# Optimization experiments

Measured on AMD Instinct MI355X. Metric: run time of the kernel, lower is better.

## Reference

```python
import jax, jax.numpy as jnp
import numpy as np

N = 100000   # nodes
G = 128      # graphs for mean pool


def gcn_conv(x, edge_index, W, b, num_nodes):
    # PyG GCNConv (default): x' = D^-1/2 (A+I) D^-1/2 (x W) + b
    x = x @ W
    src, dst = edge_index[0], edge_index[1]
    loop = jnp.arange(num_nodes)
    src = jnp.concatenate([src, loop])
    dst = jnp.concatenate([dst, loop])
    ones = jnp.ones(src.shape[0], x.dtype)
    deg = jax.ops.segment_sum(ones, dst, num_segments=num_nodes)
    dinv = jnp.where(deg > 0, jax.lax.rsqrt(deg), 0.0)
    norm = dinv[src] * dinv[dst]            # [E+N]
    msg = x[src] * norm[:, None]            # gather + scale
    out = jax.ops.segment_sum(msg, dst, num_segments=num_nodes)  # scatter-add
    return out + b


def setup_inputs() -> dict:
    key = jax.random.key(0)
    ks = jax.random.split(key, 5)
    x = jax.random.normal(ks[0], (N, 128), jnp.float32)
    edge_index = jax.random.randint(ks[1], (2, 1600000), 0, N)
    batch = jnp.sort(jax.random.randint(ks[2], (N,), 0, G))
    W1 = jax.random.normal(ks[3], (128, 64), jnp.float32) / np.sqrt(128.0)
    b1 = jnp.zeros((64,), jnp.float32)
    W2 = jax.random.normal(ks[4], (64, 64), jnp.float32) / np.sqrt(64.0)
    b2 = jnp.zeros((64,), jnp.float32)
    return {"x": x, "edge_index": edge_index, "batch": batch,
            "W1": W1, "b1": b1, "W2": W2, "b2": b2}


def reference(x, edge_index, batch, W1, b1, W2, b2):
    h = gcn_conv(x, edge_index, W1, b1, N)
    h = jax.nn.relu(h)  # dropout is identity in eval mode
    h = gcn_conv(h, edge_index, W2, b2, N)
    # global_mean_pool over graph ids
    s = jax.ops.segment_sum(h, batch, num_segments=G)
    cnt = jax.ops.segment_sum(jnp.ones((N,), h.dtype), batch, num_segments=G)
    return s / jnp.maximum(cnt, 1.0)[:, None]   # [G, hidden2]
```

## Files before the change

### kernel.cpp

```cpp
#include <hip/hip_runtime.h>
#include <hip/hip_fp16.h>

#define SLOTS 64

__global__ __launch_bounds__(256) void fill_pad(const int* __restrict__ src,
                                                const int* __restrict__ dst, int E, int N,
                                                int* __restrict__ deg,
                                                int* __restrict__ colpad, int chunks) {
  int range = blockIdx.x & 7;
  int chunk = blockIdx.x >> 3;
  int per = (N + 7) >> 3;
  int lo = range * per, hi = min(N, lo + per);
  int e0 = (int)((long long)chunk * E / chunks);
  int e1 = (int)((long long)(chunk + 1) * E / chunks);
  for (int e = e0 + (int)threadIdx.x; e < e1; e += 256) {
    int d = dst[e];
    if (d >= lo && d < hi) {
      int p = atomicAdd(&deg[d], 1);
      if (p < SLOTS) colpad[(size_t)p * N + d] = src[e];
    }
  }
}

__global__ __launch_bounds__(256) void calc_dinv(const int* __restrict__ deg,
                                                 float* __restrict__ dinv, int N) {
  int i = blockIdx.x * 256 + threadIdx.x;
  if (i < N) dinv[i] = rsqrtf((float)(deg[i] + 1));
}

template <int K, typename Tin>
__global__ __launch_bounds__(256) void gemm_dinv(const Tin* __restrict__ in,
                                                 const float* __restrict__ W,
                                                 const float* __restrict__ dinv,
                                                 __half* __restrict__ out, int N, int tiles) {
  constexpr int K4 = K / 4;
  __shared__ float4 Ws4[64][K4];
  __shared__ float Xs[32][K];
  int t = threadIdx.x;
  for (int j = t; j < 64 * K4; j += 256) {
    int c = j / K4, k4 = j % K4;
    float4 v;
    v.x = W[(4 * k4 + 0) * 64 + c];
    v.y = W[(4 * k4 + 1) * 64 + c];
    v.z = W[(4 * k4 + 2) * 64 + c];
    v.w = W[(4 * k4 + 3) * 64 + c];
    Ws4[c][k4 ^ (c & 7)] = v;
  }
  __syncthreads();
  int c0 = t & 31, rg = t >> 5;
  for (int tile = blockIdx.x; tile < tiles; tile += gridDim.x) {
    int row0 = tile * 32;
    if constexpr (sizeof(Tin) == 4) {
      for (int j = t; j < 32 * K4; j += 256) {
        int r = j / K4, k4 = j % K4;
        int rr = row0 + r;
        float4 v = (rr < N) ? *(const float4*)&in[(size_t)rr * K + 4 * k4]
                            : make_float4(0.f, 0.f, 0.f, 0.f);
        *(float4*)&Xs[r][4 * k4] = v;
      }
    } else {
      for (int j = t; j < 32 * (K / 2); j += 256) {
        int r = j / (K / 2), kk = j % (K / 2);
        int rr = row0 + r;
        float2 v = make_float2(0.f, 0.f);
        if (rr < N) {
          __half2 h = *(const __half2*)&in[(size_t)rr * K + 2 * kk];
          v = __half22float2(h);
        }
        Xs[r][2 * kk] = v.x;
        Xs[r][2 * kk + 1] = v.y;
      }
    }
    __syncthreads();
    float acc[4][2];
#pragma unroll
    for (int r = 0; r < 4; ++r) { acc[r][0] = 0.f; acc[r][1] = 0.f; }
#pragma unroll 4
    for (int k4 = 0; k4 < K4; ++k4) {
      float4 w0 = Ws4[c0][k4 ^ (c0 & 7)];
      float4 w1 = Ws4[c0 + 32][k4 ^ (c0 & 7)];
#pragma unroll
      for (int r = 0; r < 4; ++r) {
        float4 xv = *(const float4*)&Xs[rg * 4 + r][4 * k4];
        acc[r][0] = fmaf(xv.w, w0.w, fmaf(xv.z, w0.z, fmaf(xv.y, w0.y, fmaf(xv.x, w0.x, acc[r][0]))));
        acc[r][1] = fmaf(xv.w, w1.w, fmaf(xv.z, w1.z, fmaf(xv.y, w1.y, fmaf(xv.x, w1.x, acc[r][1]))));
      }
    }
#pragma unroll
    for (int r = 0; r < 4; ++r) {
      int row = row0 + rg * 4 + r;
      if (row < N) {
        float s = dinv[row];
        out[(size_t)row * 64 + c0]      = __float2half(acc[r][0] * s);
        out[(size_t)row * 64 + c0 + 32] = __float2half(acc[r][1] * s);
      }
    }
    __syncthreads();
  }
}

__global__ __launch_bounds__(256) void aggregate(const __half* __restrict__ g,
                                                 const int* __restrict__ deg_arr,
                                                 const int* __restrict__ colpad,
                                                 const float* __restrict__ dinv,
                                                 const float* __restrict__ bias,
                                                 const int* __restrict__ batch,
                                                 __half* __restrict__ out,
                                                 float* __restrict__ poolsum,
                                                 float* __restrict__ poolcnt,
                                                 int N, int mode) {
  int lane = threadIdx.x & 63;
  int wave = blockIdx.x * 4 + (threadIdx.x >> 6);
  int nwaves = gridDim.x * 4;
  int per = (N + nwaves - 1) / nwaves;
  int n0 = wave * per, n1 = min(N, n0 + per);
  if (n0 >= n1) return;
  float b = bias[lane];
  int cur = mode ? batch[n0] : 0;
  float pacc = 0.f, pcnt = 0.f;
  const int* myplane = colpad + (size_t)lane * N;
  for (int node = n0; node < n1; ++node) {
    int deg = min(deg_arr[node], SLOTS);
    int nb = (lane < deg) ? myplane[node] : 0;
    float a0 = __half2float(g[(size_t)node * 64 + lane]);
    float a1 = 0.f, a2 = 0.f, a3 = 0.f;
    float a4 = 0.f, a5 = 0.f, a6 = 0.f, a7 = 0.f;
    int j = 0;
    for (; j + 7 < deg; j += 8) {
      int s0 = __shfl(nb, j, 64);
      int s1 = __shfl(nb, j + 1, 64);
      int s2 = __shfl(nb, j + 2, 64);
      int s3 = __shfl(nb, j + 3, 64);
      int s4 = __shfl(nb, j + 4, 64);
      int s5 = __shfl(nb, j + 5, 64);
      int s6 = __shfl(nb, j + 6, 64);
      int s7 = __shfl(nb, j + 7, 64);
      a0 += __half2float(g[(size_t)s0 * 64 + lane]);
      a1 += __half2float(g[(size_t)s1 * 64 + lane]);
      a2 += __half2float(g[(size_t)s2 * 64 + lane]);
      a3 += __half2float(g[(size_t)s3 * 64 + lane]);
      a4 += __half2float(g[(size_t)s4 * 64 + lane]);
      a5 += __half2float(g[(size_t)s5 * 64 + lane]);
      a6 += __half2float(g[(size_t)s6 * 64 + lane]);
      a7 += __half2float(g[(size_t)s7 * 64 + lane]);
    }
    for (; j + 3 < deg; j += 4) {
      int s0 = __shfl(nb, j, 64);
      int s1 = __shfl(nb, j + 1, 64);
      int s2 = __shfl(nb, j + 2, 64);
      int s3 = __shfl(nb, j + 3, 64);
      a0 += __half2float(g[(size_t)s0 * 64 + lane]);
      a1 += __half2float(g[(size_t)s1 * 64 + lane]);
      a2 += __half2float(g[(size_t)s2 * 64 + lane]);
      a3 += __half2float(g[(size_t)s3 * 64 + lane]);
    }
    for (; j < deg; ++j) a0 += __half2float(g[(size_t)__shfl(nb, j, 64) * 64 + lane]);
    float r = dinv[node] * (((a0 + a1) + (a2 + a3)) + ((a4 + a5) + (a6 + a7))) + b;
    if (mode == 0) {
      out[(size_t)node * 64 + lane] = __float2half(fmaxf(r, 0.f));
    } else {
      int bg = batch[node];
      if (bg != cur) {
        atomicAdd(&poolsum[cur * 64 + lane], pacc);
        if (lane == 0) atomicAdd(&poolcnt[cur], pcnt);
        pacc = 0.f; pcnt = 0.f; cur = bg;
      }
      pacc += r; pcnt += 1.f;
    }
  }
  if (mode) {
    atomicAdd(&poolsum[cur * 64 + lane], pacc);
    if (lane == 0) atomicAdd(&poolcnt[cur], pcnt);
  }
}

__global__ __launch_bounds__(256) void finalize(const float* __restrict__ poolsum,
                                                const float* __restrict__ poolcnt,
                                                float* __restrict__ out, int Gn) {
  int i = blockIdx.x * 256 + threadIdx.x;
  if (i < Gn * 64) {
    float c = poolcnt[i >> 6];
    out[i] = poolsum[i] / fmaxf(c, 1.f);
  }
}

extern "C" void kernel_launch(void* const* d_in, const int* in_sizes, int n_in,
                              void* d_out, int out_size, void* d_ws, size_t ws_size,
                              hipStream_t stream) {
  const float* x   = (const float*)d_in[0];
  const int* ei    = (const int*)d_in[1];
  const int* batch = (const int*)d_in[2];
  const float* W1  = (const float*)d_in[3];
  const float* b1  = (const float*)d_in[4];
  const float* W2  = (const float*)d_in[5];
  const float* b2  = (const float*)d_in[6];
  float* out = (float*)d_out;

  int N  = in_sizes[2];
  int E  = in_sizes[1] / 2;
  int Gn = out_size / 64;

  char* ws = (char*)d_ws;
  size_t off = 0;
  auto alloc = [&](size_t bytes) -> void* {
    void* p = ws + off;
    off = (off + bytes + 255) & ~(size_t)255;
    return p;
  };
  int* deg       = (int*)alloc(4ull * N);
  float* poolsum = (float*)alloc(4ull * Gn * 64);
  float* poolcnt = (float*)alloc(4ull * Gn);
  size_t zero_bytes = off;
  int* colpad    = (int*)alloc(4ull * (size_t)N * SLOTS);
  float* dinv    = (float*)alloc(4ull * N);
  __half* gbuf   = (__half*)alloc(2ull * (size_t)N * 64);
  __half* ybuf   = (__half*)alloc(2ull * (size_t)N * 64);
  (void)ws_size; (void)n_in;

  hipMemsetAsync(d_ws, 0, zero_bytes, stream);

  const int* srcv = ei;
  const int* dstv = ei + E;
  int tiles = (N + 31) / 32;

  fill_pad<<<8 * 256, 256, 0, stream>>>(srcv, dstv, E, N, deg, colpad, 256);
  calc_dinv<<<(N + 255) / 256, 256, 0, stream>>>(deg, dinv, N);

  gemm_dinv<128, float><<<1536, 256, 0, stream>>>(x, W1, dinv, gbuf, N, tiles);
  aggregate<<<2048, 256, 0, stream>>>(gbuf, deg, colpad, dinv, b1, batch, ybuf,
                                      nullptr, nullptr, N, 0);
  gemm_dinv<64, __half><<<1536, 256, 0, stream>>>(ybuf, W2, dinv, gbuf, N, tiles);
  aggregate<<<2048, 256, 0, stream>>>(gbuf, deg, colpad, dinv, b2, batch, nullptr,
                                      poolsum, poolcnt, N, 1);
  finalize<<<(Gn * 64 + 255) / 256, 256, 0, stream>>>(poolsum, poolcnt, out, Gn);
}
```

Measured before the change: 366.4 us.

## Replace scalar FP32 GEMM with fp16 MFMA 16x16x32 matrix-core kernel

Rewrites the dense feature-transform kernel to use the fp16 MFMA intrinsic instead of per-thread scalar FMA loops. The input rows and the transposed weights are staged in LDS as fp16 with padded rows, and each wave computes a 16x64 output slab. The tile grows to 64 rows and the launch uses one block per tile. The fp32 input features are now rounded to fp16 before the multiply, which lowers precision. The output stores are narrower scalar half writes with a different lane mapping.

Result: faster. 311.9 us (-14.9%).

```diff
diff --git a/kernel.cpp b/kernel.cpp
--- a/kernel.cpp
+++ b/kernel.cpp
@@ -2,6 +2,9 @@
 #include <hip/hip_fp16.h>
 
 #define SLOTS 64
+
+typedef _Float16 half8 __attribute__((ext_vector_type(8)));
+typedef float f32x4 __attribute__((ext_vector_type(4)));
 
 __global__ __launch_bounds__(256) void fill_pad(const int* __restrict__ src,
                                                 const int* __restrict__ dst, int E, int N,
@@ -29,70 +32,68 @@
 }
 
 template <int K, typename Tin>
-__global__ __launch_bounds__(256) void gemm_dinv(const Tin* __restrict__ in,
+__global__ __launch_bounds__(256) void gemm_mfma(const Tin* __restrict__ in,
                                                  const float* __restrict__ W,
                                                  const float* __restrict__ dinv,
-                                                 __half* __restrict__ out, int N, int tiles) {
-  constexpr int K4 = K / 4;
-  __shared__ float4 Ws4[64][K4];
-  __shared__ float Xs[32][K];
+                                                 __half* __restrict__ out,
+                                                 int N, int tiles) {
+  constexpr int LDK = K + 8;
+  __shared__ __align__(16) _Float16 As[64][LDK];
+  __shared__ __align__(16) _Float16 Wt[64][LDK];
   int t = threadIdx.x;
-  for (int j = t; j < 64 * K4; j += 256) {
-    int c = j / K4, k4 = j % K4;
-    float4 v;
-    v.x = W[(4 * k4 + 0) * 64 + c];
-    v.y = W[(4 * k4 + 1) * 64 + c];
-    v.z = W[(4 * k4 + 2) * 64 + c];
-    v.w = W[(4 * k4 + 3) * 64 + c];
-    Ws4[c][k4 ^ (c & 7)] = v;
-  }
-  __syncthreads();
-  int c0 = t & 31, rg = t >> 5;
+  for (int j = t; j < K * 64; j += 256) {
+    int k = j >> 6, c = j & 63;
+    Wt[c][k] = (_Float16)W[j];
+  }
+  int wave = t >> 6, lane = t & 63;
+  int arow = lane & 15;
+  int kgrp = lane >> 4;
+  constexpr int C8 = K / 8;
+
   for (int tile = blockIdx.x; tile < tiles; tile += gridDim.x) {
-    int row0 = tile * 32;
-    if constexpr (sizeof(Tin) == 4) {
-      for (int j = t; j < 32 * K4; j += 256) {
-        int r = j / K4, k4 = j % K4;
-        int rr = row0 + r;
-        float4 v = (rr < N) ? *(const float4*)&in[(size_t)rr * K + 4 * k4]
-                            : make_float4(0.f, 0.f, 0.f, 0.f);
-        *(float4*)&Xs[r][4 * k4] = v;
-      }
-    } else {
-      for (int j = t; j < 32 * (K / 2); j += 256) {
-        int r = j / (K / 2), kk = j % (K / 2);
-        int rr = row0 + r;
-        float2 v = make_float2(0.f, 0.f);
+    int row0 = tile * 64;
+    for (int j = t; j < 64 * C8; j += 256) {
+      int r = j / C8, k8 = (j % C8) * 8;
+      int rr = row0 + r;
+      if constexpr (sizeof(Tin) == 4) {
+        half8 h = (half8)((_Float16)0.f);
         if (rr < N) {
-          __half2 h = *(const __half2*)&in[(size_t)rr * K + 2 * kk];
-          v = __half22float2(h);
+          float4 v0 = *(const float4*)&in[(size_t)rr * K + k8];
+          float4 v1 = *(const float4*)&in[(size_t)rr * K + k8 + 4];
+          h[0] = (_Float16)v0.x; h[1] = (_Float16)v0.y;
+          h[2] = (_Float16)v0.z; h[3] = (_Float16)v0.w;
+          h[4] = (_Float16)v1.x; h[5] = (_Float16)v1.y;
+          h[6] = (_Float16)v1.z; h[7] = (_Float16)v1.w;
         }
-        Xs[r][2 * kk] = v.x;
-        Xs[r][2 * kk + 1] = v.y;
+        *(half8*)&As[r][k8] = h;
+      } else {
+        float4 v = make_float4(0.f, 0.f, 0.f, 0.f);
+        if (rr < N) v = *(const float4*)&in[(size_t)rr * K + k8];
+        *(float4*)&As[r][k8] = v;
       }
     }
     __syncthreads();
-    float acc[4][2];
-#pragma unroll
-    for (int r = 0; r < 4; ++r) { acc[r][0] = 0.f; acc[r][1] = 0.f; }
-#pragma unroll 4
-    for (int k4 = 0; k4 < K4; ++k4) {
-      float4 w0 = Ws4[c0][k4 ^ (c0 & 7)];
-      float4 w1 = Ws4[c0 + 32][k4 ^ (c0 & 7)];
+    f32x4 acc[4];
+#pragma unroll
+    for (int ct = 0; ct < 4; ++ct) acc[ct] = (f32x4)(0.f);
+#pragma unroll
+    for (int kk = 0; kk < K; kk += 32) {
+      half8 a = *(const half8*)&As[wave * 16 + arow][kk + kgrp * 8];
+#pragma unroll
+      for (int ct = 0; ct < 4; ++ct) {
+        half8 b = *(const half8*)&Wt[ct * 16 + arow][kk + kgrp * 8];
+        acc[ct] = __builtin_amdgcn_mfma_f32_16x16x32_f16(a, b, acc[ct], 0, 0, 0);
+      }
+    }
+#pragma unroll
+    for (int ct = 0; ct < 4; ++ct) {
 #pragma unroll
       for (int r = 0; r < 4; ++r) {
-        float4 xv = *(const float4*)&Xs[rg * 4 + r][4 * k4];
-        acc[r][0] = fmaf(xv.w, w0.w, fmaf(xv.z, w0.z, fmaf(xv.y, w0.y, fmaf(xv.x, w0.x, acc[r][0]))));
-        acc[r][1] = fmaf(xv.w, w1.w, fmaf(xv.z, w1.z, fmaf(xv.y, w1.y, fmaf(xv.x, w1.x, acc[r][1]))));
-      }
-    }
-#pragma unroll
-    for (int r = 0; r < 4; ++r) {
-      int row = row0 + rg * 4 + r;
-      if (row < N) {
-        float s = dinv[row];
-        out[(size_t)row * 64 + c0]      = __float2half(acc[r][0] * s);
-        out[(size_t)row * 64 + c0 + 32] = __float2half(acc[r][1] * s);
+        int row = row0 + wave * 16 + kgrp * 4 + r;
+        if (row < N) {
+          int col = ct * 16 + arow;
+          out[(size_t)row * 64 + col] = __float2half(acc[ct][r] * dinv[row]);
+        }
       }
     }
     __syncthreads();
@@ -221,15 +222,15 @@
 
   const int* srcv = ei;
   const int* dstv = ei + E;
-  int tiles = (N + 31) / 32;
+  int tiles64 = (N + 63) / 64;
 
   fill_pad<<<8 * 256, 256, 0, stream>>>(srcv, dstv, E, N, deg, colpad, 256);
   calc_dinv<<<(N + 255) / 256, 256, 0, stream>>>(deg, dinv, N);
 
-  gemm_dinv<128, float><<<1536, 256, 0, stream>>>(x, W1, dinv, gbuf, N, tiles);
+  gemm_mfma<128, float><<<tiles64, 256, 0, stream>>>(x, W1, dinv, gbuf, N, tiles64);
   aggregate<<<2048, 256, 0, stream>>>(gbuf, deg, colpad, dinv, b1, batch, ybuf,
                                       nullptr, nullptr, N, 0);
-  gemm_dinv<64, __half><<<1536, 256, 0, stream>>>(ybuf, W2, dinv, gbuf, N, tiles);
+  gemm_mfma<64, __half><<<tiles64, 256, 0, stream>>>(ybuf, W2, dinv, gbuf, N, tiles64);
   aggregate<<<2048, 256, 0, stream>>>(gbuf, deg, colpad, dinv, b2, batch, nullptr,
                                       poolsum, poolcnt, N, 1);
   finalize<<<(Gn * 64 + 255) / 256, 256, 0, stream>>>(poolsum, poolcnt, out, Gn);
```
